# Performance work log

Hardware: AMD Instinct MI355X
Metric: run time of the kernel (lower is better)

The kernel has to match this reference:

```python
import jax, jax.numpy as jnp
import numpy as np
from math import factorial

# ---------------- real Wigner-3j coefficients (l <= 2) ----------------

def _w3j_c(l1, l2, l3, m1, m2, m3):
    if m1 + m2 + m3 != 0:
        return 0.0
    f = factorial
    pref = ((-1.0) ** (l1 - l2 - m3)) * np.sqrt(
        f(l1 + l2 - l3) * f(l1 - l2 + l3) * f(-l1 + l2 + l3) / f(l1 + l2 + l3 + 1)
        * f(l1 + m1) * f(l1 - m1) * f(l2 + m2) * f(l2 - m2) * f(l3 + m3) * f(l3 - m3))
    s = 0.0
    for t in range(0, l1 + l2 - l3 + 1):
        ds = [t, l3 - l2 + t + m1, l3 - l1 + t - m2, l1 + l2 - l3 - t, l1 - t - m1, l2 - t + m2]
        if min(ds) < 0:
            continue
        den = 1
        for d in ds:
            den *= f(d)
        s += ((-1.0) ** t) / den
    return pref * s

def _u_real(l):
    # complex->real spherical-harmonic change of basis (rows: mu=-l..l, cols: m=-l..l)
    U = np.zeros((2 * l + 1, 2 * l + 1), dtype=np.complex128)
    U[l, l] = 1.0
    for m in range(1, l + 1):
        U[l + m, l + m] = ((-1) ** m) / np.sqrt(2)
        U[l + m, l - m] = 1.0 / np.sqrt(2)
        U[l - m, l - m] = 1j / np.sqrt(2)
        U[l - m, l + m] = -1j * ((-1) ** m) / np.sqrt(2)
    return U

def _real_w3j(l1, l2, l3):
    W = np.zeros((2 * l1 + 1, 2 * l2 + 1, 2 * l3 + 1), dtype=np.complex128)
    for a, m1 in enumerate(range(-l1, l1 + 1)):
        for b, m2 in enumerate(range(-l2, l2 + 1)):
            for c, m3 in enumerate(range(-l3, l3 + 1)):
                W[a, b, c] = _w3j_c(l1, l2, l3, m1, m2, m3)
    C = np.einsum('am,bn,co,mno->abc', _u_real(l1), _u_real(l2), _u_real(l3), W)
    C = C.real + C.imag  # each entry is purely real or purely imaginary
    n = np.linalg.norm(C)
    if n > 0:
        C = C / n
    return jnp.asarray(C, dtype=jnp.float32)

W3J = {(l1, l2, l3): _real_w3j(l1, l2, l3)
       for l1 in range(3) for l2 in range(3) for l3 in range(3)
       if abs(l1 - l2) <= l3 <= l1 + l2}

SH_OFF = [0, 1, 4]
RELU_GAIN = float(np.sqrt(2.0))  # normalize2mom gain for ReLU

# ---------------- building blocks ----------------

def tp_instructions(in_ls):
    # input irrep blocks have parity (-1)**l (0e,1o,2e); sh = 0e+1o+2e; out = 0e+1o+2e
    ins = []
    for i1, l1 in enumerate(in_ls):
        for l2 in range(3):
            for l3 in range(3):
                if abs(l1 - l2) <= l3 <= l1 + l2 and ((-1) ** (l1 + l2)) == (-1) ** l3:
                    ins.append((i1, l1, l2, l3))
    return ins

def sh_l2(d):
    # component-normalized real spherical harmonics of unit vectors, l=0..2
    x, y, z = d[:, 0], d[:, 1], d[:, 2]
    s3, s15, s5 = np.sqrt(3.0), np.sqrt(15.0), np.sqrt(5.0)
    sh0 = jnp.ones_like(x)[:, None]
    sh1 = jnp.stack([s3 * y, s3 * z, s3 * x], axis=1)
    sh2 = jnp.stack([s15 * x * y, s15 * y * z, (s5 / 2) * (3 * z * z - 1.0),
                     s15 * x * z, (s15 / 2) * (x * x - y * y)], axis=1)
    return jnp.concatenate([sh0, sh1, sh2], axis=1)

def radial_basis(d, num=11, start=0.0, end=8.0):
    values = jnp.linspace(start, end, num)
    step = values[1] - values[0]
    diff = (d[:, None] - values) / step
    return jnp.exp(-(diff * diff)) / 1.12  # e3nn soft_one_hot_linspace 'gaussian'

def radial_net(rb, w1, w2):
    h = jax.nn.relu(rb @ (w1 / np.sqrt(w1.shape[0]))) * RELU_GAIN
    return h @ (w2 / np.sqrt(w2.shape[0]))

def equiv_conv(pos, x, src, dst, rw1, rw2, in_ls, mul_in, C):
    E = src.shape[0]
    vec = pos[src] - pos[dst]                      # (E,3)
    dist = jnp.sqrt(jnp.sum(vec * vec, axis=1))    # (E,)
    w = radial_net(radial_basis(dist), rw1, rw2)   # (E, weight_numel)
    dirs = vec / jnp.maximum(dist, 1e-12)[:, None]
    sh = sh_l2(dirs)                               # (E,9)
    xd = x[dst]                                    # edge gather
    ins = tp_instructions(in_ls)
    fan = {0: 0, 1: 0, 2: 0}
    for (_, l1, l2, l3) in ins:
        fan[l3] += mul_in
    in_off = np.cumsum([0] + [mul_in * (2 * l + 1) for l in in_ls])
    out = [jnp.zeros((E, C, 2 * l3 + 1), x.dtype) for l3 in range(3)]
    woff = 0
    for (i1, l1, l2, l3) in ins:
        x1 = xd[:, in_off[i1]:in_off[i1 + 1]].reshape(E, mul_in, 2 * l1 + 1)
        shb = sh[:, SH_OFF[l2]:SH_OFF[l2] + 2 * l2 + 1]
        wi = w[:, woff:woff + mul_in * C].reshape(E, mul_in, C)
        woff += mul_in * C
        alpha = np.sqrt(2 * l3 + 1) / np.sqrt(fan[l3])
        out[l3] = out[l3] + alpha * jnp.einsum('eui,ej,euw,ijk->ewk', x1, shb, wi, W3J[(l1, l2, l3)])
    msg = jnp.concatenate([o.reshape(E, -1) for o in out], axis=1)
    return jax.ops.segment_sum(msg, src, num_segments=pos.shape[0])  # scatter_add onto src

def self_interaction(x, W, mul_in):
    # x: mul_in x (0e+1o+2e); W: (3, mul_in, mul_out)
    outs, off = [], 0
    for l in range(3):
        d = 2 * l + 1
        b = x[:, off:off + mul_in * d].reshape(-1, mul_in, d)
        off += mul_in * d
        outs.append((jnp.einsum('nui,uw->nwi', b, W[l]) / np.sqrt(mul_in)).reshape(x.shape[0], -1))
    return jnp.concatenate(outs, axis=1)

def pointwise_nonlin(x, b, mul):
    outs, off = [], 0
    for l in range(3):
        d = 2 * l + 1
        blk = x[:, off:off + mul * d]
        off += mul * d
        if l == 0:
            outs.append(jax.nn.softplus(blk + b[0]))
        else:
            v = blk.reshape(-1, mul, d)
            gate = jax.nn.softplus(jnp.sqrt(jnp.sum(v * v, axis=2) + 1e-24) + b[l])
            outs.append((v * gate[:, :, None]).reshape(x.shape[0], -1))
    return jnp.concatenate(outs, axis=1)

def pointwise_norm(x):
    return x / (jnp.linalg.norm(x, axis=1, keepdims=True) + 1e-6)

def backbone(pos, features, edge_index, si0_w, c1_rw1, c1_rw2, si1_w, nl1_b,
             c2_rw1, c2_rw2, si2_w, nl2_b, c3_rw1, c3_rw2, si3_w, nl3_b, fsi_w):
    src, dst = edge_index[0], edge_index[1]
    x = features @ si0_w / np.sqrt(features.shape[1])          # 64x0e -> 128x0e
    x = equiv_conv(pos, x, src, dst, c1_rw1, c1_rw2, [0], 128, 128)
    x = pointwise_norm(x)
    x = self_interaction(x, si1_w, 128)
    x = pointwise_nonlin(x, nl1_b, 128)
    x = equiv_conv(pos, x, src, dst, c2_rw1, c2_rw2, [0, 1, 2], 128, 64)
    x = pointwise_norm(x)
    x = self_interaction(x, si2_w, 64)
    x = pointwise_nonlin(x, nl2_b, 64)
    x = equiv_conv(pos, x, src, dst, c3_rw1, c3_rw2, [0, 1, 2], 64, 32)
    x = pointwise_norm(x)
    x = self_interaction(x, si3_w, 32)
    x = pointwise_nonlin(x, nl3_b, 32)
    x = self_interaction(x, fsi_w, 32)
    return x[:, :32]  # scalar (0e) part

# ---------------- harness ----------------

N_NODES, N_EDGES, FEAT = 512, 2048, 64

def setup_inputs() -> dict:
    key = jax.random.key(0)
    ks = jax.random.split(key, 20)
    src = jax.random.randint(ks[0], (N_EDGES,), 0, N_NODES)
    # avoid self-loops (zero-length edges are degenerate for normalize/grad)
    dst = (src + 1 + jax.random.randint(ks[1], (N_EDGES,), 0, N_NODES - 1)) % N_NODES
    edge_index = jnp.stack([src, dst]).astype(jnp.int64)
    rn = lambda k, s: jax.random.normal(k, s, dtype=jnp.float32)
    return {
        'pos': rn(ks[2], (N_NODES, 3)),
        'features': rn(ks[3], (N_NODES, FEAT)),
        'edge_index': edge_index,
        'si0_w': rn(ks[4], (FEAT, 128)),
        'c1_rw1': rn(ks[5], (11, 12)), 'c1_rw2': rn(ks[6], (12, 3 * 128 * 128)),
        'si1_w': rn(ks[7], (3, 128, 128)), 'nl1_b': jnp.zeros((3,), jnp.float32),
        'c2_rw1': rn(ks[8], (11, 12)), 'c2_rw2': rn(ks[9], (12, 11 * 128 * 64)),
        'si2_w': rn(ks[10], (3, 64, 64)), 'nl2_b': jnp.zeros((3,), jnp.float32),
        'c3_rw1': rn(ks[11], (11, 12)), 'c3_rw2': rn(ks[12], (12, 11 * 64 * 32)),
        'si3_w': rn(ks[13], (3, 32, 32)), 'nl3_b': jnp.zeros((3,), jnp.float32),
        'fsi_w': rn(ks[14], (3, 32, 32)),
    }

def reference(pos, features, edge_index, si0_w, c1_rw1, c1_rw2, si1_w, nl1_b,
              c2_rw1, c2_rw2, si2_w, nl2_b, c3_rw1, c3_rw2, si3_w, nl3_b, fsi_w):
    return backbone(pos, features, edge_index, si0_w, c1_rw1, c1_rw2, si1_w, nl1_b,
                    c2_rw1, c2_rw2, si2_w, nl2_b, c3_rw1, c3_rw2, si3_w, nl3_b, fsi_w)
```

## Files before the change

### kernel.cpp

```cpp
#include <hip/hip_runtime.h>
#include <cmath>
#include <cstdint>

#define NNODES 512
#define NEDGES 2048

typedef _Float16 half2v __attribute__((ext_vector_type(2)));

#define OFF_W3J   0
#define OFF_SH    512
#define OFF_H1    (OFF_SH + NEDGES*9)
#define OFF_H2    (OFF_H1 + NEDGES*6)
#define OFF_H3    (OFF_H2 + NEDGES*6)
#define OFF_W2P1  (OFF_H3 + NEDGES*6)
#define OFF_W2P2  (OFF_W2P1 + 6*49152)
#define OFF_W2P3  (OFF_W2P2 + 6*90112)
#define OFF_XH    (OFF_W2P3 + 6*22528)
#define OFF_XB    (OFF_XH + NNODES*576)
#define OFF_MSGA  (OFF_XB + NNODES*1152)
#define OFF_CNT   (OFF_MSGA + NEDGES*576)
#define OFF_COFF  (OFF_CNT + 512)
#define OFF_LIST  (OFF_COFF + 1024)
#define OFF_RANK  (OFF_LIST + 2048)
#define OFF_MSGB  (OFF_RANK + 2048)
#define WS_NEED_SPLIT ((size_t)(OFF_MSGB + NEDGES*576) * 4)

__device__ __forceinline__ unsigned int packh2f(float a, float b){
  half2v h; h.x=(_Float16)a; h.y=(_Float16)b;
  return __builtin_bit_cast(unsigned int, h);
}
__device__ __forceinline__ half2v u2h2(unsigned int u){ return __builtin_bit_cast(half2v, u); }
__device__ __forceinline__ float dot2f(unsigned int a, unsigned int b, float c){
#if __has_builtin(__builtin_amdgcn_fdot2)
  return __builtin_amdgcn_fdot2(u2h2(a), u2h2(b), c, false);
#else
  half2v ha=u2h2(a), hb=u2h2(b);
  return c + (float)ha.x*(float)hb.x + (float)ha.y*(float)hb.y;
#endif
}
__device__ __forceinline__ unsigned int pk2(float a, float b){
#if __has_builtin(__builtin_amdgcn_cvt_pkrtz)
  auto h=__builtin_amdgcn_cvt_pkrtz(a,b);
  return __builtin_bit_cast(unsigned int,h);
#else
  return packh2f(a,b);
#endif
}
__device__ __forceinline__ unsigned short f2h(float f){
  _Float16 h=(_Float16)f; return __builtin_bit_cast(unsigned short,h);
}
__device__ __forceinline__ float softplusf(float v){ return fmaxf(v,0.f)+log1pf(expf(-fabsf(v))); }

__device__ double dfact(int n){ double f=1.0; for(int i=2;i<=n;++i) f*=(double)i; return f; }

__device__ double w3j_c_dev(int l1,int l2,int l3,int m1,int m2,int m3){
  if (m1+m2+m3 != 0) return 0.0;
  int p = l1 - l2 - m3;
  double sign = (((p%2)+2)%2) ? -1.0 : 1.0;
  double pref = sign*sqrt(dfact(l1+l2-l3)*dfact(l1-l2+l3)*dfact(-l1+l2+l3)/dfact(l1+l2+l3+1)
              *dfact(l1+m1)*dfact(l1-m1)*dfact(l2+m2)*dfact(l2-m2)*dfact(l3+m3)*dfact(l3-m3));
  double s=0.0;
  for (int t=0;t<=l1+l2-l3;++t){
    int d0=t, d1v=l3-l2+t+m1, d2v=l3-l1+t-m2, d3v=l1+l2-l3-t, d4=l1-t-m1, d5=l2-t+m2;
    if (d0<0||d1v<0||d2v<0||d3v<0||d4<0||d5<0) continue;
    double den=dfact(d0)*dfact(d1v)*dfact(d2v)*dfact(d3v)*dfact(d4)*dfact(d5);
    s += ((t&1)?-1.0:1.0)/den;
  }
  return pref*s;
}

__device__ void u_real_dev(int l, double Ur[5][5], double Ui[5][5]){
  for(int a=0;a<5;++a)for(int b=0;b<5;++b){Ur[a][b]=0.0;Ui[a][b]=0.0;}
  Ur[l][l]=1.0;
  double inv2 = 1.0/sqrt(2.0);
  for(int m=1;m<=l;++m){
    double sgn = (m&1)?-1.0:1.0;
    Ur[l+m][l+m] = sgn*inv2;
    Ur[l+m][l-m] = inv2;
    Ui[l-m][l-m] = inv2;
    Ui[l-m][l+m] = -sgn*inv2;
  }
}

__global__ void w3j_kernel(float* __restrict__ out){
  const int L1[11]={0,0,0,1,1,1,1,2,2,2,2};
  const int L2[11]={0,1,2,0,1,1,2,0,1,2,2};
  const int L3[11]={0,1,2,1,0,2,1,2,1,0,2};
  const int OFF[11]={0,1,10,35,44,53,98,143,168,213,238};
  int t = blockIdx.x;
  int tid = threadIdx.x;
  int l1=L1[t], l2=L2[t], l3=L3[t];
  int d1=2*l1+1, d2=2*l2+1, d3=2*l3+1;
  int sz=d1*d2*d3;
  __shared__ double Wt[125];
  __shared__ double U1r[5][5],U1i[5][5],U2r[5][5],U2i[5][5],U3r[5][5],U3i[5][5];
  __shared__ double Cv[125];
  __shared__ double red[128];
  for(int idx=tid; idx<sz; idx+=128){
    int a=idx/(d2*d3), rem=idx%(d2*d3), b=rem/d3, c=rem%d3;
    Wt[idx]=w3j_c_dev(l1,l2,l3,a-l1,b-l2,c-l3);
  }
  if(tid==0) u_real_dev(l1,U1r,U1i);
  if(tid==1) u_real_dev(l2,U2r,U2i);
  if(tid==2) u_real_dev(l3,U3r,U3i);
  __syncthreads();
  for(int idx=tid; idx<sz; idx+=128){
    int a=idx/(d2*d3), rem=idx%(d2*d3), b=rem/d3, c=rem%d3;
    double cr=0.0, ci=0.0;
    for(int m=0;m<d1;++m)for(int n=0;n<d2;++n){
      double t2r = U1r[a][m]*U2r[b][n]-U1i[a][m]*U2i[b][n];
      double t2i = U1r[a][m]*U2i[b][n]+U1i[a][m]*U2r[b][n];
      if (t2r==0.0 && t2i==0.0) continue;
      for(int o=0;o<d3;++o){
        double wv=Wt[(m*d2+n)*d3+o];
        if (wv==0.0) continue;
        double t3r=t2r*U3r[c][o]-t2i*U3i[c][o];
        double t3i=t2r*U3i[c][o]+t2i*U3r[c][o];
        cr += t3r*wv; ci += t3i*wv;
      }
    }
    Cv[idx]=cr+ci;
  }
  __syncthreads();
  double s=0.0;
  for(int idx=tid; idx<sz; idx+=128) s+=Cv[idx]*Cv[idx];
  red[tid]=s; __syncthreads();
  for(int d=64; d>0; d>>=1){ if(tid<d) red[tid]+=red[tid+d]; __syncthreads(); }
  double nrm = sqrt(red[0]);
  double inv = (nrm>0.0)?1.0/nrm:0.0;
  for(int idx=tid; idx<sz; idx+=128) out[OFF[t]+idx]=(float)(Cv[idx]*inv);
}

__global__ void edge_prep_kernel(const float* __restrict__ pos, const int* __restrict__ ei,
    const float* __restrict__ rw1a, const float* __restrict__ rw1b, const float* __restrict__ rw1c,
    float* __restrict__ sh, unsigned int* __restrict__ h1, unsigned int* __restrict__ h2,
    unsigned int* __restrict__ h3){
  int e = blockIdx.x*blockDim.x+threadIdx.x;
  if (e>=NEDGES) return;
  int s = ei[e], d = ei[NEDGES+e];
  float vx=pos[3*s]-pos[3*d], vy=pos[3*s+1]-pos[3*d+1], vz=pos[3*s+2]-pos[3*d+2];
  float dist=sqrtf(vx*vx+vy*vy+vz*vz);
  float dm = fmaxf(dist,1e-12f);
  float x=vx/dm, y=vy/dm, z=vz/dm;
  const float s3=sqrtf(3.f), s15=sqrtf(15.f), s5=sqrtf(5.f);
  float shv[9];
  shv[0]=1.f; shv[1]=s3*y; shv[2]=s3*z; shv[3]=s3*x;
  shv[4]=s15*x*y; shv[5]=s15*y*z; shv[6]=0.5f*s5*(3.f*z*z-1.f); shv[7]=s15*x*z; shv[8]=0.5f*s15*(x*x-y*y);
  #pragma unroll
  for(int i=0;i<9;++i) sh[e*9+i]=shv[i];
  float rb[11];
  #pragma unroll
  for(int i=0;i<11;++i){ float diff=(dist-0.8f*(float)i)*(1.f/0.8f); rb[i]=expf(-diff*diff)*(1.f/1.12f); }
  const float c1 = 1.f/sqrtf(11.f);
  const float c2 = sqrtf(2.f)/sqrtf(12.f);
  const float* rws[3]={rw1a,rw1b,rw1c};
  unsigned int* outs[3]={h1,h2,h3};
  for(int L=0;L<3;++L){
    float hv[12];
    #pragma unroll
    for(int r=0;r<12;++r){
      float t=0.f;
      #pragma unroll
      for(int k=0;k<11;++k) t+=rb[k]*rws[L][k*12+r];
      t*=c1;
      hv[r]=fmaxf(t,0.f)*c2;
    }
    #pragma unroll
    for(int r2=0;r2<6;++r2) outs[L][e*6+r2]=packh2f(hv[2*r2],hv[2*r2+1]);
  }
}

__global__ void w2pack_kernel(const float* __restrict__ w2, unsigned int* __restrict__ out, int nW){
  int idx=blockIdx.x*256+threadIdx.x;
  if(idx>=6*nW) return;
  int r2=idx/nW, c=idx-r2*nW;
  out[idx]=packh2f(w2[(size_t)(2*r2)*nW+c], w2[(size_t)(2*r2+1)*nW+c]);
}

__global__ void w1pack_kernel(const float* __restrict__ w2, unsigned int* __restrict__ out){
  int idx=blockIdx.x*256+threadIdx.x;
  if(idx>=384*768) return;
  int col=idx/768, rem=idx-col*768;
  int r=rem/64, u2=rem-r*64;
  int i=col>>7, w=col&127;
  size_t s0=(size_t)r*49152 + i*16384 + (2*u2)*128 + w;
  out[idx]=packh2f(w2[s0], w2[s0+128]);
}

__global__ __launch_bounds__(384) void vgemm1_kernel(const unsigned int* __restrict__ xh,
    const unsigned int* __restrict__ w1p, unsigned int* __restrict__ V){
  __shared__ __align__(16) unsigned int s_x[4][64];
  int tid=threadIdx.x;
  int n0=blockIdx.x*4;
  for(int ix=tid; ix<256; ix+=384){ int n=ix>>6, u2=ix&63; s_x[n][u2]=xh[(size_t)(n0+n)*64+u2]; }
  __syncthreads();
  int col=tid;
  float acc[4][12];
  #pragma unroll
  for(int n=0;n<4;++n)
    #pragma unroll
    for(int r=0;r<12;++r) acc[n][r]=0.f;
  const uint4* Wp=(const uint4*)(w1p + (size_t)col*768);
  for(int u4=0;u4<16;++u4){
    uint4 xv[4];
    #pragma unroll
    for(int n=0;n<4;++n) xv[n]=((const uint4*)s_x[n])[u4];
    #pragma unroll
    for(int r=0;r<12;++r){
      uint4 wv=Wp[r*16+u4];
      #pragma unroll
      for(int n=0;n<4;++n){
        acc[n][r]=dot2f(xv[n].x,wv.x,acc[n][r]);
        acc[n][r]=dot2f(xv[n].y,wv.y,acc[n][r]);
        acc[n][r]=dot2f(xv[n].z,wv.z,acc[n][r]);
        acc[n][r]=dot2f(xv[n].w,wv.w,acc[n][r]);
      }
    }
  }
  #pragma unroll
  for(int n=0;n<4;++n)
    #pragma unroll
    for(int r2=0;r2<6;++r2)
      V[((size_t)(n0+n)*384+col)*6+r2]=pk2(acc[n][2*r2],acc[n][2*r2+1]);
}

__global__ __launch_bounds__(384) void conv1_edge_kernel(const unsigned int* __restrict__ V,
    const unsigned int* __restrict__ h1, const float* __restrict__ shb,
    const int* __restrict__ dstp, const float* __restrict__ w3j,
    unsigned int* __restrict__ msgA){
  const int W3O[3]={0,1,10};
  unsigned short* m16=(unsigned short*)msgA;
  int tid=threadIdx.x;
  int col=tid;
  int i=col>>7, w=col&127;
  int d3=2*i+1;
  float alpha=sqrtf((float)(2*i+1))*(1.f/sqrtf(128.f));
  int e0=blockIdx.x*2;
  #pragma unroll
  for(int s=0;s<2;++s){
    int e=e0+s;
    int n=dstp[e];
    const unsigned int* vp=V+((size_t)n*384+col)*6;
    float G=0.f;
    #pragma unroll
    for(int r2=0;r2<6;++r2) G=dot2f(h1[(size_t)e*6+r2], vp[r2], G);
    int base=(i==0)?0:((i==1)?128:512);
    for(int k=0;k<d3;++k){
      float B=0.f;
      for(int j=0;j<d3;++j) B += shb[(size_t)e*9+i*i+j]*w3j[W3O[i]+j*d3+k];
      m16[(size_t)e*1152 + base + w*d3 + k]=f2h(G*B*alpha);
    }
  }
}

__global__ __launch_bounds__(256) void csr_rank_kernel(const int* __restrict__ src,
    int* __restrict__ cnt, int* __restrict__ rankA){
  __shared__ int s_src[NEDGES];
  int tid=threadIdx.x;
  int4* s4=(int4*)s_src;
  const int4* g4=(const int4*)src;
  for(int i=tid;i<NEDGES/4;i+=256) s4[i]=g4[i];
  __syncthreads();
  int e=blockIdx.x*256+tid;
  int s=s_src[e];
  int lt=0, tot=0;
  for(int b=0;b<NEDGES/4;b+=8){
    int4 v[8];
    #pragma unroll
    for(int k=0;k<8;++k) v[k]=s4[b+k];
    #pragma unroll
    for(int k=0;k<8;++k){
      int j0=4*(b+k);
      tot += ((v[k].x==s)?1:0)+((v[k].y==s)?1:0)+((v[k].z==s)?1:0)+((v[k].w==s)?1:0);
      lt  += ((v[k].x==s&&j0<e)?1:0)+((v[k].y==s&&j0+1<e)?1:0)+((v[k].z==s&&j0+2<e)?1:0)+((v[k].w==s&&j0+3<e)?1:0);
    }
  }
  rankA[e]=lt;
  if(lt==tot-1) cnt[s]=tot;
}

__global__ void csr_scan_kernel(const int* __restrict__ cnt, int* __restrict__ coff){
  __shared__ int s[NNODES];
  int tid=threadIdx.x;
  s[tid]=cnt[tid];
  __syncthreads();
  for(int d=1;d<NNODES;d<<=1){
    int v=(tid>=d)?s[tid-d]:0;
    __syncthreads();
    s[tid]+=v;
    __syncthreads();
  }
  coff[tid+1]=s[tid];
  if(tid==0) coff[0]=0;
}

__global__ void csr_scatter_kernel(const int* __restrict__ src, const int* __restrict__ coff,
    const int* __restrict__ rankA, int* __restrict__ list){
  int e=blockIdx.x*256+threadIdx.x;
  int s=src[e];
  list[coff[s]+rankA[e]]=e;
}

__global__ void si0_kernel(const float* __restrict__ feat, const float* __restrict__ w,
                           unsigned int* __restrict__ xh){
  __shared__ float s_f[64];
  __shared__ unsigned short s_v[128];
  int n=blockIdx.x, tid=threadIdx.x;
  if(tid<64) s_f[tid]=feat[n*64+tid];
  __syncthreads();
  float acc=0.f;
  for(int u=0;u<64;++u) acc += s_f[u]*w[u*128+tid];
  s_v[tid]=f2h(acc*0.125f);
  __syncthreads();
  if(tid<64) xh[(size_t)n*64+tid]=((unsigned int)s_v[2*tid+1]<<16)|s_v[2*tid];
}

struct CInstr { int l1,l2,l3,woff,w3off; float alpha; };
struct LayerArg { CInstr ins[3][4]; int cnt[3]; int gOf[8]; int rank[8]; int nxg[3]; };

template<int MUL,int C,int EB,int NL,int USPLIT,int D3,int L1v>
__device__ __forceinline__ void instr_body(
  const unsigned int* __restrict__ W2h, int nW, int woff,
  const unsigned int (&hreg)[EB][6],
  const uint4* s_xp4, const float* sB,
  float (&acc)[EB][D3], int ubase, int uOff2, int w)
{
  constexpr int D1=2*L1v+1;
  constexpr int MULZ=MUL/USPLIT;
  constexpr int MZ2=MULZ/2;
  constexpr int UC=256/C;
  constexpr int CHZ=MUL/(UC*USPLIT);
  constexpr int CB=(L1v==0)?0:((L1v==1)?MZ2:4*MZ2);
  static_assert(EB==4,"EB must be 4");
  static_assert(CHZ>=2 && (CHZ&1)==0,"CHZ even");
  const unsigned int* Wp = W2h + (size_t)woff + (size_t)ubase*C + w;
  float a2[EB][D1];
  #pragma unroll
  for(int e=0;e<EB;++e){
    #pragma unroll
    for(int i=0;i<D1;++i) a2[e][i]=0.f;
  }
  #pragma unroll 2
  for(int u2=0;u2<CHZ/2;++u2){
    unsigned int wv0[6],wv1[6];
    #pragma unroll
    for(int r=0;r<6;++r){
      wv0[r]=Wp[(size_t)r*nW + (size_t)(2*u2)*C];
      wv1[r]=Wp[(size_t)r*nW + (size_t)(2*u2+1)*C];
    }
    unsigned int wi2[EB];
    #pragma unroll
    for(int e=0;e<EB;++e){
      float w0=0.f,w1=0.f;
      #pragma unroll
      for(int r=0;r<6;++r){ w0=dot2f(hreg[e][r],wv0[r],w0); w1=dot2f(hreg[e][r],wv1[r],w1); }
      wi2[e]=pk2(w0,w1);
    }
    #pragma unroll
    for(int i=0;i<D1;++i){
      uint4 xv = s_xp4[CB + i*MZ2 + uOff2 + u2];
      a2[0][i]=dot2f(wi2[0],xv.x,a2[0][i]);
      a2[1][i]=dot2f(wi2[1],xv.y,a2[1][i]);
      a2[2][i]=dot2f(wi2[2],xv.z,a2[2][i]);
      a2[3][i]=dot2f(wi2[3],xv.w,a2[3][i]);
    }
  }
  #pragma unroll
  for(int e=0;e<EB;++e){
    #pragma unroll
    for(int k=0;k<D3;++k){
      float s=0.f;
      #pragma unroll
      for(int i=0;i<D1;++i) s += a2[e][i]*sB[e*25+i*5+k];
      acc[e][k]+=s;
    }
  }
}

template<int MUL,int C,int EB,int NL,int USPLIT,int D3,int NINS>
__device__ __forceinline__ void conv_main(
  const unsigned int* __restrict__ W2h, int nW,
  const unsigned int (&hreg)[EB][6],
  const uint4* s_xp4, const float* s_B, float* s_red, unsigned short* s_msg,
  unsigned int* __restrict__ msg, const LayerArg& la, int g, int e0,
  int w, int uc, int ubase, int uOff2)
{
  constexpr int UC=256/C;
  const int tid=threadIdx.x;
  float acc[EB][D3];
  #pragma unroll
  for(int e=0;e<EB;++e){
    #pragma unroll
    for(int k=0;k<D3;++k) acc[e][k]=0.f;
  }
  #pragma unroll
  for(int ii=0;ii<NINS;++ii){
    const int l1v=la.ins[g][ii].l1;
    const int woff=la.ins[g][ii].woff;
    switch(l1v){
      case 0: instr_body<MUL,C,EB,NL,USPLIT,D3,0>(W2h,nW,woff,hreg,s_xp4,s_B+ii*EB*25,acc,ubase,uOff2,w); break;
      case 1: instr_body<MUL,C,EB,NL,USPLIT,D3,1>(W2h,nW,woff,hreg,s_xp4,s_B+ii*EB*25,acc,ubase,uOff2,w); break;
      default: instr_body<MUL,C,EB,NL,USPLIT,D3,2>(W2h,nW,woff,hreg,s_xp4,s_B+ii*EB*25,acc,ubase,uOff2,w); break;
    }
  }
  constexpr int L3v=(D3-1)/2;
  constexpr int base32=(L3v==0)?0:((L3v==1)?C/2:2*C);
  constexpr int seg32=C*D3/2;
  for(int e=0;e<EB;++e){
    #pragma unroll
    for(int k=0;k<D3;++k) s_red[k*256+tid]=acc[e][k];
    __syncthreads();
    if(uc==0){
      #pragma unroll
      for(int k=0;k<D3;++k){
        float s=0.f;
        #pragma unroll
        for(int c2=0;c2<UC;++c2) s+=s_red[k*256+c2*C+w];
        s_msg[(e*C+w)*D3+k]=f2h(s);
      }
    }
    __syncthreads();
  }
  const unsigned int* sm32=(const unsigned int*)s_msg;
  for(int ix=tid; ix<EB*seg32; ix+=256){
    int e=ix/seg32, o=ix-e*seg32;
    msg[(size_t)(e0+e)*(9*C/2) + base32 + o] = sm32[e*seg32+o];
  }
}

template<int MUL,int C,int EB,int NL,int USPLIT>
__global__ __launch_bounds__(256,4) void conv_kernel(
  const unsigned int* __restrict__ xh, const unsigned int* __restrict__ W2h, int nW,
  const unsigned int* __restrict__ hb, const float* __restrict__ shb,
  const int* __restrict__ dstp, const float* __restrict__ w3j,
  unsigned int* __restrict__ msg0, unsigned int* __restrict__ msg1, LayerArg la)
{
  constexpr int MUL2=MUL/2;
  constexpr int MULZ=MUL/USPLIT;
  constexpr int MZ2=MULZ/2;
  constexpr int ROW=(NL==1)?MUL2:9*MUL2;
  constexpr int SROW=(NL==1)?MZ2:9*MZ2;
  constexpr int UC=256/C;
  constexpr int CHZ=MUL/(UC*USPLIT);
  constexpr int NB=NEDGES/EB;
  __shared__ unsigned int s_xp[SROW*EB];
  __shared__ float s_B[4*EB*25];
  __shared__ float s_red[5*256];
  __shared__ unsigned short s_msg[EB*C*5];
  int tid=threadIdx.x;
  int bid=blockIdx.x;
  int xcd=bid&7, slot=bid>>3;
  int g=la.gOf[xcd];
  int idx=slot*la.nxg[g]+la.rank[xcd];
  if(idx>=NB*USPLIT) return;
  int zz=idx/NB, et=idx-zz*NB;
  int e0=et*EB;
  unsigned int* msg=(zz==0)?msg0:msg1;
  for(int ix=tid; ix<EB*SROW; ix+=256){
    int e=ix/SROW, c=ix-(ix/SROW)*SROW;
    int l1,i,u2l;
    if(NL==1){ l1=0;i=0;u2l=c; }
    else{
      if(c<MZ2){l1=0;i=0;u2l=c;}
      else if(c<4*MZ2){int t=c-MZ2;i=t/MZ2;u2l=t-i*MZ2;l1=1;}
      else{int t=c-4*MZ2;i=t/MZ2;u2l=t-i*MZ2;l1=2;}
    }
    int gb=(l1==0)?0:((l1==1)?MUL2:4*MUL2);
    int dn=dstp[e0+e];
    s_xp[c*EB+e]=xh[(size_t)dn*ROW + gb + i*MUL2 + zz*MZ2 + u2l];
  }
  int nIns=la.cnt[g];
  for(int ix=tid; ix<nIns*EB*25; ix+=256){
    int ii=ix/(EB*25); int rem=ix%(EB*25); int e=rem/25; int q=rem%25;
    int i=q/5,k=q%5;
    CInstr I=la.ins[g][ii];
    int d1=2*I.l1+1,d2=2*I.l2+1,d3v=2*I.l3+1;
    float v=0.f;
    if(i<d1&&k<d3v){
      int sho=I.l2*I.l2;
      for(int j=0;j<d2;++j) v+=shb[(size_t)(e0+e)*9+sho+j]*w3j[I.w3off+(i*d2+j)*d3v+k];
      v*=I.alpha;
    }
    s_B[(ii*EB+e)*25+q]=v;
  }
  __syncthreads();
  int w=tid%C, uc=tid/C;
  int ubase=zz*MULZ+uc*CHZ;
  int uOff2=uc*(CHZ/2);
  unsigned int hreg[EB][6];
  #pragma unroll
  for(int e=0;e<EB;++e){
    #pragma unroll
    for(int r=0;r<6;++r) hreg[e][r]=hb[(size_t)(e0+e)*6+r];
  }
  const uint4* s_xp4=(const uint4*)s_xp;
  if(NL==1){
    if(g==0)      conv_main<MUL,C,EB,NL,USPLIT,1,1>(W2h,nW,hreg,s_xp4,s_B,s_red,s_msg,msg,la,g,e0,w,uc,ubase,uOff2);
    else if(g==1) conv_main<MUL,C,EB,NL,USPLIT,3,1>(W2h,nW,hreg,s_xp4,s_B,s_red,s_msg,msg,la,g,e0,w,uc,ubase,uOff2);
    else          conv_main<MUL,C,EB,NL,USPLIT,5,1>(W2h,nW,hreg,s_xp4,s_B,s_red,s_msg,msg,la,g,e0,w,uc,ubase,uOff2);
  }else{
    if(g==0)      conv_main<MUL,C,EB,NL,USPLIT,1,3>(W2h,nW,hreg,s_xp4,s_B,s_red,s_msg,msg,la,g,e0,w,uc,ubase,uOff2);
    else if(g==1) conv_main<MUL,C,EB,NL,USPLIT,3,4>(W2h,nW,hreg,s_xp4,s_B,s_red,s_msg,msg,la,g,e0,w,uc,ubase,uOff2);
    else          conv_main<MUL,C,EB,NL,USPLIT,5,4>(W2h,nW,hreg,s_xp4,s_B,s_red,s_msg,msg,la,g,e0,w,uc,ubase,uOff2);
  }
}

template<int MUL>
__global__ void agg_post_kernel(const unsigned int* __restrict__ msg0,
                                const unsigned int* __restrict__ msg1,
                                const int* __restrict__ coff, const int* __restrict__ list,
                                const float* __restrict__ siw, const float* __restrict__ nlb,
                                unsigned int* __restrict__ xh){
  constexpr int W32=MUL*9/2;
  constexpr int ROW=9*MUL/2;
  __shared__ float s_in[MUL*9];
  __shared__ unsigned short s_out[MUL*9];
  __shared__ float red[256];
  int n=blockIdx.x, tid=threadIdx.x;
  int b=coff[n], en=coff[n+1];
  float ss=0.f;
  for(int c32=tid;c32<W32;c32+=256){
    float a0=0.f,a1=0.f;
    for(int j=b;j<en;++j){
      size_t o=(size_t)list[j]*W32+c32;
      half2v p=u2h2(msg0[o]); a0+=(float)p.x; a1+=(float)p.y;
      if(msg1){ half2v q=u2h2(msg1[o]); a0+=(float)q.x; a1+=(float)q.y; }
    }
    s_in[2*c32]=a0; s_in[2*c32+1]=a1;
    ss+=a0*a0+a1*a1;
  }
  red[tid]=ss; __syncthreads();
  for(int d=128;d>0;d>>=1){ if(tid<d) red[tid]+=red[tid+d]; __syncthreads(); }
  float scale=1.f/(sqrtf(red[0])+1e-6f);
  const float inv=scale/sqrtf((float)MUL);
  float b0=nlb[0], b1=nlb[1], b2=nlb[2];
  for(int p=tid;p<3*MUL;p+=256){
    int l=p/MUL, wo=p%MUL;
    if(l==0){
      const float* Wl=siw;
      float a=0.f;
      for(int u=0;u<MUL;++u) a+=s_in[u]*Wl[(size_t)u*MUL+wo];
      s_out[wo]=f2h(softplusf(a*inv+b0));
    } else if(l==1){
      const float* Wl=siw+(size_t)MUL*MUL;
      float v0=0.f,v1=0.f,v2=0.f;
      for(int u=0;u<MUL;++u){
        float wv=Wl[(size_t)u*MUL+wo];
        int bi=MUL+u*3;
        v0+=s_in[bi]*wv; v1+=s_in[bi+1]*wv; v2+=s_in[bi+2]*wv;
      }
      v0*=inv; v1*=inv; v2*=inv;
      float gate=softplusf(sqrtf(v0*v0+v1*v1+v2*v2+1e-24f)+b1);
      int ob=MUL+wo*3;
      s_out[ob]=f2h(v0*gate); s_out[ob+1]=f2h(v1*gate); s_out[ob+2]=f2h(v2*gate);
    } else {
      const float* Wl=siw+(size_t)2*MUL*MUL;
      float v0=0.f,v1=0.f,v2=0.f,v3=0.f,v4=0.f;
      for(int u=0;u<MUL;++u){
        float wv=Wl[(size_t)u*MUL+wo];
        int bi=4*MUL+u*5;
        v0+=s_in[bi]*wv; v1+=s_in[bi+1]*wv; v2+=s_in[bi+2]*wv; v3+=s_in[bi+3]*wv; v4+=s_in[bi+4]*wv;
      }
      v0*=inv; v1*=inv; v2*=inv; v3*=inv; v4*=inv;
      float gate=softplusf(sqrtf(v0*v0+v1*v1+v2*v2+v3*v3+v4*v4+1e-24f)+b2);
      int ob=4*MUL+wo*5;
      s_out[ob]=f2h(v0*gate); s_out[ob+1]=f2h(v1*gate); s_out[ob+2]=f2h(v2*gate);
      s_out[ob+3]=f2h(v3*gate); s_out[ob+4]=f2h(v4*gate);
    }
  }
  __syncthreads();
  for(int p=tid;p<ROW;p+=256){
    int l,i,u2;
    if(p<MUL/2){l=0;i=0;u2=p;}
    else if(p<2*MUL){int t=p-MUL/2;i=t/(MUL/2);u2=t%(MUL/2);l=1;}
    else{int t=p-2*MUL;i=t/(MUL/2);u2=t%(MUL/2);l=2;}
    int d=2*l+1, sb=MUL*l*l;
    unsigned short a=s_out[sb+(2*u2)*d+i], bb=s_out[sb+(2*u2+1)*d+i];
    xh[(size_t)n*ROW+p]=((unsigned int)bb<<16)|a;
  }
}

__global__ void final_kernel(const unsigned int* __restrict__ xh, const float* __restrict__ fsi,
                             float* __restrict__ out){
  int gid=blockIdx.x*blockDim.x+threadIdx.x;
  if(gid>=NNODES*32) return;
  int n=gid/32, wo=gid%32;
  float s=0.f;
  for(int u2=0;u2<16;++u2){
    half2v p=u2h2(xh[(size_t)n*144+u2]);
    s += (float)p.x*fsi[(2*u2)*32+wo] + (float)p.y*fsi[(2*u2+1)*32+wo];
  }
  out[gid]=s*(1.f/sqrtf(32.f));
}

static int w3off_of(int l1,int l2,int l3){
  const int L1[11]={0,0,0,1,1,1,1,2,2,2,2};
  const int L2[11]={0,1,2,0,1,1,2,0,1,2,2};
  const int L3[11]={0,1,2,1,0,2,1,2,1,0,2};
  const int OFF[11]={0,1,10,35,44,53,98,143,168,213,238};
  for(int i=0;i<11;++i) if(L1[i]==l1&&L2[i]==l2&&L3[i]==l3) return OFF[i];
  return 0;
}

static void fill_map(LayerArg& la, const int alloc[3]){
  int x=0;
  for(int g=0;g<3;++g){
    la.nxg[g]=alloc[g];
    for(int r=0;r<alloc[g];++r){ la.gOf[x]=g; la.rank[x]=r; ++x; }
  }
}
static int gridS(const int alloc[3], int NBZ){
  int S=0;
  for(int g=0;g<3;++g){ int s=(NBZ+alloc[g]-1)/alloc[g]; if(s>S)S=s; }
  return S;
}

extern "C" void kernel_launch(void* const* d_in, const int* in_sizes, int n_in,
                              void* d_out, int out_size, void* d_ws, size_t ws_size,
                              hipStream_t stream) {
  const float* pos    = (const float*)d_in[0];
  const float* feat   = (const float*)d_in[1];
  const int*   ei     = (const int*)d_in[2];
  const float* si0w   = (const float*)d_in[3];
  const float* c1_rw1 = (const float*)d_in[4];
  const float* c1_rw2 = (const float*)d_in[5];
  const float* si1w   = (const float*)d_in[6];
  const float* nl1b   = (const float*)d_in[7];
  const float* c2_rw1 = (const float*)d_in[8];
  const float* c2_rw2 = (const float*)d_in[9];
  const float* si2w   = (const float*)d_in[10];
  const float* nl2b   = (const float*)d_in[11];
  const float* c3_rw1 = (const float*)d_in[12];
  const float* c3_rw2 = (const float*)d_in[13];
  const float* si3w   = (const float*)d_in[14];
  const float* nl3b   = (const float*)d_in[15];
  const float* fsiw   = (const float*)d_in[16];

  float* ws_f=(float*)d_ws;
  float* w3   = ws_f+OFF_W3J;
  float* sh   = ws_f+OFF_SH;
  unsigned int* h1   = (unsigned int*)(ws_f+OFF_H1);
  unsigned int* h2   = (unsigned int*)(ws_f+OFF_H2);
  unsigned int* h3   = (unsigned int*)(ws_f+OFF_H3);
  unsigned int* w2p1 = (unsigned int*)(ws_f+OFF_W2P1);
  unsigned int* w2p2 = (unsigned int*)(ws_f+OFF_W2P2);
  unsigned int* w2p3 = (unsigned int*)(ws_f+OFF_W2P3);
  unsigned int* xh   = (unsigned int*)(ws_f+OFF_XH);
  unsigned int* msgA = (unsigned int*)(ws_f+OFF_MSGA);
  unsigned int* msgB = (unsigned int*)(ws_f+OFF_MSGB);
  unsigned int* V    = msgB;
  int* cnt    = (int*)(ws_f+OFF_CNT);
  int* coff   = (int*)(ws_f+OFF_COFF);
  int* clist  = (int*)(ws_f+OFF_LIST);
  int* rankA  = (int*)(ws_f+OFF_RANK);
  const int* src  = ei;
  const int* dstp = ei+NEDGES;

  const bool split = ws_size >= WS_NEED_SPLIT;
  const int NB = NEDGES/4;

  LayerArg la1{}, la2{}, la3{};
  {
    int step=128*128;
    for(int i=0;i<3;++i){
      CInstr I{0,i,i, i*step, w3off_of(0,i,i), (float)std::sqrt((2.0*i+1.0)/128.0)};
      la1.ins[i][la1.cnt[i]++]=I;
    }
  }
  const int insL[11][3]={{0,0,0},{0,1,1},{0,2,2},{1,0,1},{1,1,0},{1,1,2},{1,2,1},{2,0,2},{2,1,1},{2,2,0},{2,2,2}};
  auto build=[&](LayerArg& la, int mul, int Cc){
    int step=mul*Cc;
    int fan[3]={0,0,0};
    for(int i=0;i<11;++i) fan[insL[i][2]] += mul;
    for(int i=0;i<11;++i){
      int l1v=insL[i][0],l2v=insL[i][1],l3v=insL[i][2];
      CInstr I{l1v,l2v,l3v, i*step, w3off_of(l1v,l2v,l3v), (float)std::sqrt((2.0*l3v+1.0)/(double)fan[l3v])};
      la.ins[l3v][la.cnt[l3v]++]=I;
    }
  };
  build(la2,128,64);
  build(la3,64,32);

  const int alloc1[3]={3,3,2};
  const int alloc23[3]={2,3,3};
  fill_map(la1,alloc1);
  fill_map(la2,alloc23);
  fill_map(la3,alloc23);

  w3j_kernel<<<dim3(11),dim3(128),0,stream>>>(w3);
  edge_prep_kernel<<<dim3(NEDGES/256),dim3(256),0,stream>>>(pos,ei,c1_rw1,c2_rw1,c3_rw1, sh,h1,h2,h3);
  if(split){
    w1pack_kernel<<<dim3((384*768+255)/256),dim3(256),0,stream>>>(c1_rw2,w2p1);
  } else {
    w2pack_kernel<<<dim3((6*49152+255)/256),dim3(256),0,stream>>>(c1_rw2,w2p1,49152);
  }
  w2pack_kernel<<<dim3((6*90112+255)/256),dim3(256),0,stream>>>(c2_rw2,w2p2,90112);
  w2pack_kernel<<<dim3((6*22528+255)/256),dim3(256),0,stream>>>(c3_rw2,w2p3,22528);

  hipMemsetAsync(cnt,0,NNODES*sizeof(int),stream);
  csr_rank_kernel<<<dim3(NEDGES/256),dim3(256),0,stream>>>(src,cnt,rankA);
  csr_scan_kernel<<<dim3(1),dim3(NNODES),0,stream>>>(cnt,coff);
  csr_scatter_kernel<<<dim3(NEDGES/256),dim3(256),0,stream>>>(src,coff,rankA,clist);

  si0_kernel<<<dim3(NNODES),dim3(128),0,stream>>>(feat,si0w,xh);

  if(split){
    vgemm1_kernel<<<dim3(NNODES/4),dim3(384),0,stream>>>(xh,w2p1,V);
    conv1_edge_kernel<<<dim3(NEDGES/2),dim3(384),0,stream>>>(V,h1,sh,dstp,w3,msgA);
    agg_post_kernel<128><<<dim3(NNODES),dim3(256),0,stream>>>(msgA,(const unsigned int*)nullptr,coff,clist,si1w,nl1b,xh);
    int S23=gridS(alloc23,NB*2);
    conv_kernel<128,64,4,3,2><<<dim3(8*S23),dim3(256),0,stream>>>(xh,w2p2,90112,h2,sh,dstp,w3,msgA,msgB,la2);
    agg_post_kernel<64><<<dim3(NNODES),dim3(256),0,stream>>>(msgA,msgB,coff,clist,si2w,nl2b,xh);
    int S3=gridS(alloc23,NB);
    conv_kernel<64,32,4,3,1><<<dim3(8*S3),dim3(256),0,stream>>>(xh,w2p3,22528,h3,sh,dstp,w3,msgA,msgA,la3);
    agg_post_kernel<32><<<dim3(NNODES),dim3(256),0,stream>>>(msgA,(const unsigned int*)nullptr,coff,clist,si3w,nl3b,xh);
  } else {
    int S1=gridS(alloc1,NB), S23=gridS(alloc23,NB);
    conv_kernel<128,128,4,1,1><<<dim3(8*S1),dim3(256),0,stream>>>(xh,w2p1,49152,h1,sh,dstp,w3,msgA,msgA,la1);
    agg_post_kernel<128><<<dim3(NNODES),dim3(256),0,stream>>>(msgA,(const unsigned int*)nullptr,coff,clist,si1w,nl1b,xh);
    conv_kernel<128,64,4,3,1><<<dim3(8*S23),dim3(256),0,stream>>>(xh,w2p2,90112,h2,sh,dstp,w3,msgA,msgA,la2);
    agg_post_kernel<64><<<dim3(NNODES),dim3(256),0,stream>>>(msgA,(const unsigned int*)nullptr,coff,clist,si2w,nl2b,xh);
    conv_kernel<64,32,4,3,1><<<dim3(8*S23),dim3(256),0,stream>>>(xh,w2p3,22528,h3,sh,dstp,w3,msgA,msgA,la3);
    agg_post_kernel<32><<<dim3(NNODES),dim3(256),0,stream>>>(msgA,(const unsigned int*)nullptr,coff,clist,si3w,nl3b,xh);
  }

  final_kernel<<<dim3((NNODES*32+255)/256),dim3(256),0,stream>>>(xh,fsiw,(float*)d_out);
}
```

Before: 322.8 us.

## Interleave packed radial weights per column and swizzle LDS gather layout

Repacks the half2 radial-weight tensor so the six r-pairs for each column sit contiguously, letting each thread load them with three 8-byte loads instead of six strided 4-byte loads. It also applies an XOR swizzle to the shared-memory gathered node-feature buffer, on both the write and the uint4 read, to reduce LDS bank conflicts. The per-thread loads are now strided by 24 bytes across lanes instead of unit-stride, which may hurt global coalescing. The 8-byte loads also need 8-byte alignment of woff and the per-u offsets.

```diff
diff --git a/kernel.cpp b/kernel.cpp
--- a/kernel.cpp
+++ b/kernel.cpp
@@ -50,6 +50,7 @@
   _Float16 h=(_Float16)f; return __builtin_bit_cast(unsigned short,h);
 }
 __device__ __forceinline__ float softplusf(float v){ return fmaxf(v,0.f)+log1pf(expf(-fabsf(v))); }
+__device__ __forceinline__ int swz(int c){ return c ^ ((c>>3)&3); }
 
 __device__ double dfact(int n){ double f=1.0; for(int i=2;i<=n;++i) f*=(double)i; return f; }
 
@@ -173,7 +174,7 @@
 __global__ void w2pack_kernel(const float* __restrict__ w2, unsigned int* __restrict__ out, int nW){
   int idx=blockIdx.x*256+threadIdx.x;
   if(idx>=6*nW) return;
-  int r2=idx/nW, c=idx-r2*nW;
+  int c=idx/6, r2=idx-c*6;
   out[idx]=packh2f(w2[(size_t)(2*r2)*nW+c], w2[(size_t)(2*r2+1)*nW+c]);
 }
 
@@ -320,7 +321,7 @@
 
 template<int MUL,int C,int EB,int NL,int USPLIT,int D3,int L1v>
 __device__ __forceinline__ void instr_body(
-  const unsigned int* __restrict__ W2h, int nW, int woff,
+  const unsigned int* __restrict__ W2h, int woff,
   const unsigned int (&hreg)[EB][6],
   const uint4* s_xp4, const float* sB,
   float (&acc)[EB][D3], int ubase, int uOff2, int w)
@@ -333,7 +334,7 @@
   constexpr int CB=(L1v==0)?0:((L1v==1)?MZ2:4*MZ2);
   static_assert(EB==4,"EB must be 4");
   static_assert(CHZ>=2 && (CHZ&1)==0,"CHZ even");
-  const unsigned int* Wp = W2h + (size_t)woff + (size_t)ubase*C + w;
+  const unsigned int* Wp = W2h + (size_t)(woff + ubase*C + w)*6;
   float a2[EB][D1];
   #pragma unroll
   for(int e=0;e<EB;++e){
@@ -342,12 +343,12 @@
   }
   #pragma unroll 2
   for(int u2=0;u2<CHZ/2;++u2){
-    unsigned int wv0[6],wv1[6];
-    #pragma unroll
-    for(int r=0;r<6;++r){
-      wv0[r]=Wp[(size_t)r*nW + (size_t)(2*u2)*C];
-      wv1[r]=Wp[(size_t)r*nW + (size_t)(2*u2+1)*C];
-    }
+    const uint2* qa=(const uint2*)(Wp + (size_t)(2*u2)*C*6);
+    const uint2* qb=(const uint2*)(Wp + (size_t)(2*u2+1)*C*6);
+    uint2 a0=qa[0], a1=qa[1], a2q=qa[2];
+    uint2 b0=qb[0], b1=qb[1], b2q=qb[2];
+    unsigned int wv0[6]={a0.x,a0.y,a1.x,a1.y,a2q.x,a2q.y};
+    unsigned int wv1[6]={b0.x,b0.y,b1.x,b1.y,b2q.x,b2q.y};
     unsigned int wi2[EB];
     #pragma unroll
     for(int e=0;e<EB;++e){
@@ -358,7 +359,7 @@
     }
     #pragma unroll
     for(int i=0;i<D1;++i){
-      uint4 xv = s_xp4[CB + i*MZ2 + uOff2 + u2];
+      uint4 xv = s_xp4[swz(CB + i*MZ2 + uOff2 + u2)];
       a2[0][i]=dot2f(wi2[0],xv.x,a2[0][i]);
       a2[1][i]=dot2f(wi2[1],xv.y,a2[1][i]);
       a2[2][i]=dot2f(wi2[2],xv.z,a2[2][i]);
@@ -379,7 +380,7 @@
 
 template<int MUL,int C,int EB,int NL,int USPLIT,int D3,int NINS>
 __device__ __forceinline__ void conv_main(
-  const unsigned int* __restrict__ W2h, int nW,
+  const unsigned int* __restrict__ W2h,
   const unsigned int (&hreg)[EB][6],
   const uint4* s_xp4, const float* s_B, float* s_red, unsigned short* s_msg,
   unsigned int* __restrict__ msg, const LayerArg& la, int g, int e0,
@@ -398,9 +399,9 @@
     const int l1v=la.ins[g][ii].l1;
     const int woff=la.ins[g][ii].woff;
     switch(l1v){
-      case 0: instr_body<MUL,C,EB,NL,USPLIT,D3,0>(W2h,nW,woff,hreg,s_xp4,s_B+ii*EB*25,acc,ubase,uOff2,w); break;
-      case 1: instr_body<MUL,C,EB,NL,USPLIT,D3,1>(W2h,nW,woff,hreg,s_xp4,s_B+ii*EB*25,acc,ubase,uOff2,w); break;
-      default: instr_body<MUL,C,EB,NL,USPLIT,D3,2>(W2h,nW,woff,hreg,s_xp4,s_B+ii*EB*25,acc,ubase,uOff2,w); break;
+      case 0: instr_body<MUL,C,EB,NL,USPLIT,D3,0>(W2h,woff,hreg,s_xp4,s_B+ii*EB*25,acc,ubase,uOff2,w); break;
+      case 1: instr_body<MUL,C,EB,NL,USPLIT,D3,1>(W2h,woff,hreg,s_xp4,s_B+ii*EB*25,acc,ubase,uOff2,w); break;
+      default: instr_body<MUL,C,EB,NL,USPLIT,D3,2>(W2h,woff,hreg,s_xp4,s_B+ii*EB*25,acc,ubase,uOff2,w); break;
     }
   }
   constexpr int L3v=(D3-1)/2;
@@ -467,7 +468,7 @@
     }
     int gb=(l1==0)?0:((l1==1)?MUL2:4*MUL2);
     int dn=dstp[e0+e];
-    s_xp[c*EB+e]=xh[(size_t)dn*ROW + gb + i*MUL2 + zz*MZ2 + u2l];
+    s_xp[swz(c)*EB+e]=xh[(size_t)dn*ROW + gb + i*MUL2 + zz*MZ2 + u2l];
   }
   int nIns=la.cnt[g];
   for(int ix=tid; ix<nIns*EB*25; ix+=256){
@@ -495,13 +496,13 @@
   }
   const uint4* s_xp4=(const uint4*)s_xp;
   if(NL==1){
-    if(g==0)      conv_main<MUL,C,EB,NL,USPLIT,1,1>(W2h,nW,hreg,s_xp4,s_B,s_red,s_msg,msg,la,g,e0,w,uc,ubase,uOff2);
-    else if(g==1) conv_main<MUL,C,EB,NL,USPLIT,3,1>(W2h,nW,hreg,s_xp4,s_B,s_red,s_msg,msg,la,g,e0,w,uc,ubase,uOff2);
-    else          conv_main<MUL,C,EB,NL,USPLIT,5,1>(W2h,nW,hreg,s_xp4,s_B,s_red,s_msg,msg,la,g,e0,w,uc,ubase,uOff2);
+    if(g==0)      conv_main<MUL,C,EB,NL,USPLIT,1,1>(W2h,hreg,s_xp4,s_B,s_red,s_msg,msg,la,g,e0,w,uc,ubase,uOff2);
+    else if(g==1) conv_main<MUL,C,EB,NL,USPLIT,3,1>(W2h,hreg,s_xp4,s_B,s_red,s_msg,msg,la,g,e0,w,uc,ubase,uOff2);
+    else          conv_main<MUL,C,EB,NL,USPLIT,5,1>(W2h,hreg,s_xp4,s_B,s_red,s_msg,msg,la,g,e0,w,uc,ubase,uOff2);
   }else{
-    if(g==0)      conv_main<MUL,C,EB,NL,USPLIT,1,3>(W2h,nW,hreg,s_xp4,s_B,s_red,s_msg,msg,la,g,e0,w,uc,ubase,uOff2);
-    else if(g==1) conv_main<MUL,C,EB,NL,USPLIT,3,4>(W2h,nW,hreg,s_xp4,s_B,s_red,s_msg,msg,la,g,e0,w,uc,ubase,uOff2);
-    else          conv_main<MUL,C,EB,NL,USPLIT,5,4>(W2h,nW,hreg,s_xp4,s_B,s_red,s_msg,msg,la,g,e0,w,uc,ubase,uOff2);
+    if(g==0)      conv_main<MUL,C,EB,NL,USPLIT,1,3>(W2h,hreg,s_xp4,s_B,s_red,s_msg,msg,la,g,e0,w,uc,ubase,uOff2);
+    else if(g==1) conv_main<MUL,C,EB,NL,USPLIT,3,4>(W2h,hreg,s_xp4,s_B,s_red,s_msg,msg,la,g,e0,w,uc,ubase,uOff2);
+    else          conv_main<MUL,C,EB,NL,USPLIT,5,4>(W2h,hreg,s_xp4,s_B,s_red,s_msg,msg,la,g,e0,w,uc,ubase,uOff2);
   }
 }
 
```

Result: no change. 326.1 us (+1.0%).
